# Optimization experiments

Measured on AMD Instinct MI355X. Metric: run time of the kernel, lower is better.

## Reference

```python
import jax, jax.numpy as jnp
import numpy as np

B, T, LA, L = 4, 32, 32, 512
D, H, C = 2048, 16, 128
KV_DIM = 2048
K = T * LA  # total kv tokens per batch element
EPS = 1e-5


def _ln(x):
    m = jnp.mean(x, axis=-1, keepdims=True)
    v = jnp.var(x, axis=-1, keepdims=True)
    return (x - m) * jax.lax.rsqrt(v + EPS)


def setup_inputs() -> dict:
    key = jax.random.key(0)
    ks = jax.random.split(key, 10)
    s = 1.0 / np.sqrt(D)
    sk = 1.0 / np.sqrt(KV_DIM)
    return {
        "x": jax.random.normal(ks[0], (B, T, LA, KV_DIM), jnp.float32),
        "latents": jax.random.normal(ks[1], (B, L, D), jnp.float32),
        "t_emb": jax.random.normal(ks[2], (B, 3, D), jnp.float32) * 0.02,
        "q_lens": jnp.full((B,), L, dtype=jnp.int32),
        "k_lens": jax.random.randint(ks[3], (B,), K // 2, K + 1).astype(jnp.int32),
        "ln_kv_w": jnp.ones((KV_DIM,), jnp.float32),
        "ln_kv_b": jnp.zeros((KV_DIM,), jnp.float32),
        "ssg": jax.random.normal(ks[4], (1, 3, D), jnp.float32) * s,  # shift_scale_gate param (adaLN=True)
        "Wq": jax.random.normal(ks[5], (D, D), jnp.float32) * s,
        "bq": jnp.zeros((D,), jnp.float32),
        "Wkv": jax.random.normal(ks[6], (KV_DIM, 2 * D), jnp.float32) * sk,
        "bkv": jnp.zeros((2 * D,), jnp.float32),
        "Wo": jax.random.normal(ks[7], (D, D), jnp.float32) * s,
        "bo": jnp.zeros((D,), jnp.float32),
    }


def reference(x, latents, t_emb, q_lens, k_lens, ln_kv_w, ln_kv_b, ssg,
              Wq, bq, Wkv, bkv, Wo, bo):
    # norm_kv (affine LayerNorm over kv_dim)
    xk = _ln(x) * ln_kv_w + ln_kv_b  # (B,T,LA,KV_DIM)
    # AdaLN modulate: shift/scale/gate from t_emb + learned shift_scale_gate
    mod = t_emb + ssg  # (B,3,D)
    shift, scale, gate = mod[:, 0:1], mod[:, 1:2], mod[:, 2:3]  # (B,1,D)
    norm_q = _ln(latents)  # norm_q has no affine when adaLN=True
    lat = norm_q * (1.0 + scale) + shift
    # projections
    q = (lat @ Wq + bq).reshape(B, L, H, C)
    kv = (xk.reshape(B, K, KV_DIM) @ Wkv + bkv)  # (B,K,2D)
    k, v = kv[..., :D], kv[..., D:]
    k = k.reshape(B, K, H, C)
    v = v.reshape(B, K, H, C)
    # varlen attention == per-batch masked attention (keys beyond k_lens masked)
    scores = jnp.einsum("blhc,bkhc->bhlk", q, k) / np.sqrt(C)
    kmask = jnp.arange(K)[None, :] < k_lens[:, None]  # (B,K)
    scores = jnp.where(kmask[:, None, None, :], scores, jnp.finfo(scores.dtype).min)
    attn = jax.nn.softmax(scores, axis=-1)
    out = jnp.einsum("bhlk,bkhc->blhc", attn, v).reshape(B, L, D)
    # queries beyond q_lens are invalid -> zero them (varlen packing semantics)
    qmask = (jnp.arange(L)[None, :] < q_lens[:, None])[..., None]  # (B,L,1)
    out = out * qmask
    return (out @ Wo + bo) * gate
```

## Files before the change

kernel.cpp:

```cpp
#include <hip/hip_runtime.h>

typedef unsigned short u16;
typedef short bf16x8 __attribute__((ext_vector_type(8)));
typedef float f32x4 __attribute__((ext_vector_type(4)));

#define MFMA_BF16(a, b, c) __builtin_amdgcn_mfma_f32_16x16x32_bf16((a), (b), (c), 0, 0, 0)
#define ATT_SCALE 0.08838834764831845f

__device__ __forceinline__ u16 f2bf(float f) {
  union { float f; unsigned int u; } cv;
  cv.f = f;
  unsigned int u = cv.u + 0x7fffu + ((cv.u >> 16) & 1u);
  return (u16)(u >> 16);
}

__device__ __forceinline__ void gload_lds16(const u16* g, u16* l) {
  __builtin_amdgcn_global_load_lds(
      (const __attribute__((address_space(1))) unsigned int*)g,
      (__attribute__((address_space(3))) unsigned int*)l, 16, 0, 0);
}

__global__ __launch_bounds__(256) void prep_kernel(
    const float* __restrict__ x, const float* __restrict__ ln_w,
    const float* __restrict__ ln_b, const float* __restrict__ latents,
    const float* __restrict__ t_emb, const float* __restrict__ ssg,
    const float* __restrict__ Wq, const float* __restrict__ Wo,
    const float* __restrict__ Wkv,
    u16* __restrict__ xk_out, u16* __restrict__ lat_out,
    u16* __restrict__ WqT, u16* __restrict__ WoT, u16* __restrict__ WkvT)
{
  __shared__ float shmem[32 * 33];
  const int blk = blockIdx.x;
  const int tid = threadIdx.x;
  if (blk < 6144) {
    const bool is_x = blk < 4096;
    const int row = is_x ? blk : blk - 4096;
    const float* src = is_x ? (x + (size_t)row * 2048) : (latents + (size_t)row * 2048);
    const float4* xr = (const float4*)src;
    float4 v0 = xr[tid];
    float4 v1 = xr[tid + 256];
    float sum = v0.x + v0.y + v0.z + v0.w + v1.x + v1.y + v1.z + v1.w;
    float sq  = v0.x*v0.x + v0.y*v0.y + v0.z*v0.z + v0.w*v0.w
              + v1.x*v1.x + v1.y*v1.y + v1.z*v1.z + v1.w*v1.w;
    #pragma unroll
    for (int off = 32; off > 0; off >>= 1) {
      sum += __shfl_xor(sum, off);
      sq  += __shfl_xor(sq, off);
    }
    if ((tid & 63) == 0) { shmem[tid >> 6] = sum; shmem[(tid >> 6) + 4] = sq; }
    __syncthreads();
    sum = shmem[0] + shmem[1] + shmem[2] + shmem[3];
    sq  = shmem[4] + shmem[5] + shmem[6] + shmem[7];
    const float mean = sum * (1.0f / 2048.0f);
    const float var  = sq * (1.0f / 2048.0f) - mean * mean;
    const float rstd = rsqrtf(var + 1e-5f);
    if (is_x) {
      const float4* w4 = (const float4*)ln_w;
      const float4* b4 = (const float4*)ln_b;
      ushort4* orow = (ushort4*)(xk_out + (size_t)row * 2048);
      #pragma unroll
      for (int j = 0; j < 2; ++j) {
        const int idx = tid + j * 256;
        const float4 v = j ? v1 : v0;
        const float4 ww = w4[idx];
        const float4 bb = b4[idx];
        ushort4 o;
        o.x = f2bf((v.x - mean) * rstd * ww.x + bb.x);
        o.y = f2bf((v.y - mean) * rstd * ww.y + bb.y);
        o.z = f2bf((v.z - mean) * rstd * ww.z + bb.z);
        o.w = f2bf((v.w - mean) * rstd * ww.w + bb.w);
        orow[idx] = o;
      }
    } else {
      const int bidx = row >> 9;
      const float4* te = (const float4*)(t_emb + (size_t)bidx * 3 * 2048);
      const float4* sg = (const float4*)ssg;
      ushort4* orow = (ushort4*)(lat_out + (size_t)row * 2048);
      #pragma unroll
      for (int j = 0; j < 2; ++j) {
        const int idx = tid + j * 256;
        const float4 v = j ? v1 : v0;
        const float4 t0 = te[idx];
        const float4 t1 = te[512 + idx];
        const float4 s0 = sg[idx];
        const float4 s1 = sg[512 + idx];
        ushort4 o;
        o.x = f2bf(((v.x - mean) * rstd) * (1.0f + t1.x + s1.x) + (t0.x + s0.x));
        o.y = f2bf(((v.y - mean) * rstd) * (1.0f + t1.y + s1.y) + (t0.y + s0.y));
        o.z = f2bf(((v.z - mean) * rstd) * (1.0f + t1.z + s1.z) + (t0.z + s0.z));
        o.w = f2bf(((v.w - mean) * rstd) * (1.0f + t1.w + s1.w) + (t0.w + s0.w));
        orow[idx] = o;
      }
    }
  } else {
    int t = blk - 6144;
    const float* in;
    u16* outp;
    int C, cx, ry;
    if (t < 4096)      { in = Wq;  outp = WqT;  C = 2048; cx = t & 63;  ry = t >> 6; }
    else if (t < 8192) { t -= 4096; in = Wo;  outp = WoT;  C = 2048; cx = t & 63;  ry = t >> 6; }
    else               { t -= 8192; in = Wkv; outp = WkvT; C = 4096; cx = t & 127; ry = t >> 7; }
    float (*tile)[33] = (float(*)[33])shmem;
    const int R = 2048;
    const int c0 = cx * 32;
    const int r0 = ry * 32;
    const int tx = tid & 31;
    const int ty = tid >> 5;
    #pragma unroll
    for (int i = 0; i < 4; ++i)
      tile[ty + i * 8][tx] = in[(size_t)(r0 + ty + i * 8) * C + c0 + tx];
    __syncthreads();
    #pragma unroll
    for (int i = 0; i < 4; ++i)
      outp[(size_t)(c0 + ty + i * 8) * R + r0 + tx] = f2bf(tile[tx][ty + i * 8]);
  }
}

template<int BM>
__global__ __launch_bounds__(256) void gemm_bf16_kernel(
    const u16* __restrict__ A, const u16* __restrict__ BT,
    int Kd, int mode,
    const float* __restrict__ bias,
    u16* __restrict__ out_q, float* __restrict__ out_f,
    const float* __restrict__ t_emb, const float* __restrict__ ssg)
{
  constexpr int TI = BM / 32;
  __shared__ u16 As[2][BM][40];
  __shared__ u16 Bs[2][128][40];
  const int tid  = threadIdx.x;
  const int lane = tid & 63;
  const int wv   = tid >> 6;
  const int wm   = wv & 1, wn = wv >> 1;
  const int quad = lane >> 4, lq = lane & 15;
  const int m0 = blockIdx.y * BM, n0 = blockIdx.x * 128;

  f32x4 acc[TI][4];
  #pragma unroll
  for (int i = 0; i < TI; ++i)
    #pragma unroll
    for (int j = 0; j < 4; ++j)
      acc[i][j] = (f32x4){0.f, 0.f, 0.f, 0.f};

  const int rB  = tid >> 1;
  const int hfB = (tid & 1) * 16;
  const u16* gB = BT + (size_t)(n0 + rB) * Kd + hfB;
  const int rA  = (BM == 128) ? (tid >> 1) : (tid >> 2);
  const int hA  = (BM == 128) ? 0 : ((tid >> 1) & 1);
  const int hfA = (tid & 1) * 16;
  const u16* gA = A + (size_t)(m0 + rA) * Kd + hA * 32 + hfA;

  for (int k0 = 0; k0 < Kd; k0 += 64) {
    uint4 a00, a01;
    a00 = *(const uint4*)(gA + k0);
    a01 = *(const uint4*)(gA + k0 + 8);
    const uint4 b00 = *(const uint4*)(gB + k0);
    const uint4 b01 = *(const uint4*)(gB + k0 + 8);
    const uint4 b10 = *(const uint4*)(gB + k0 + 32);
    const uint4 b11 = *(const uint4*)(gB + k0 + 40);
    __syncthreads();
    *(uint4*)&As[hA][rA][hfA]     = a00;
    *(uint4*)&As[hA][rA][hfA + 8] = a01;
    *(uint4*)&Bs[0][rB][hfB]     = b00;
    *(uint4*)&Bs[0][rB][hfB + 8] = b01;
    *(uint4*)&Bs[1][rB][hfB]     = b10;
    *(uint4*)&Bs[1][rB][hfB + 8] = b11;
    __syncthreads();
    #pragma unroll
    for (int kk = 0; kk < 2; ++kk) {
      bf16x8 av[TI], bv[4];
      #pragma unroll
      for (int i = 0; i < TI; ++i)
        av[i] = *(const bf16x8*)&As[kk][wm * (BM / 2) + i * 16 + lq][quad * 8];
      #pragma unroll
      for (int j = 0; j < 4; ++j)
        bv[j] = *(const bf16x8*)&Bs[kk][wn * 64 + j * 16 + lq][quad * 8];
      #pragma unroll
      for (int i = 0; i < TI; ++i)
        #pragma unroll
        for (int j = 0; j < 4; ++j)
          acc[i][j] = MFMA_BF16(av[i], bv[j], acc[i][j]);
    }
  }

  #pragma unroll
  for (int i = 0; i < TI; ++i) {
    const int mlb = m0 + wm * (BM / 2) + i * 16 + quad * 4;
    #pragma unroll
    for (int j = 0; j < 4; ++j) {
      const int n = n0 + wn * 64 + j * 16 + lq;
      const float bs = bias[n];
      if (mode == 0) {
        const int h = n >> 7, c = n & 127;
        #pragma unroll
        for (int rr = 0; rr < 4; ++rr) {
          const int m = mlb + rr;
          const int bb = m >> 9, l = m & 511;
          out_q[((size_t)(bb * 16 + h) * 512 + l) * 128 + c] =
              f2bf((acc[i][j][rr] + bs) * ATT_SCALE);
        }
      } else {
        #pragma unroll
        for (int rr = 0; rr < 4; ++rr) {
          const int m = mlb + rr;
          const int bb = m >> 9;
          const float g = t_emb[((size_t)bb * 3 + 2) * 2048 + n] + ssg[2 * 2048 + n];
          out_f[(size_t)m * 2048 + n] = (acc[i][j][rr] + bs) * g;
        }
      }
    }
  }
}

#define KV_BARRIER() asm volatile("s_barrier" ::: "memory")

#define KV_MMA(MH, NH, BV)                                                     \
  do {                                                                         \
    _Pragma("unroll")                                                          \
    for (int i = 0; i < 4; ++i) {                                              \
      _Pragma("unroll")                                                        \
      for (int j = 0; j < 2; ++j) {                                            \
        acc[(MH)*4 + i][(NH)*2 + j] =                                          \
            MFMA_BF16(av[i][0], BV[j][0], acc[(MH)*4 + i][(NH)*2 + j]);        \
        acc[(MH)*4 + i][(NH)*2 + j] =                                          \
            MFMA_BF16(av[i][1], BV[j][1], acc[(MH)*4 + i][(NH)*2 + j]);        \
      }                                                                        \
    }                                                                          \
  } while (0)

__global__ __launch_bounds__(512, 2) void gemm_kv_8phase(
    const u16* __restrict__ A, const u16* __restrict__ BT,
    const float* __restrict__ bias,
    u16* __restrict__ out_k, u16* __restrict__ out_vT,
    const int* __restrict__ k_lens)
{
  extern __shared__ __align__(16) u16 lds[];
  u16* const Alds = lds;
  u16* const Blds = lds + 32768;

  const int tid  = threadIdx.x;
  const int lane = tid & 63;
  const int wv   = tid >> 6;
  const int wm   = wv >> 2;
  const int wn   = wv & 3;
  const int quad = lane >> 4, lq = lane & 15;
  const int m0 = blockIdx.y * 256, n0 = blockIdx.x * 256;

  f32x4 acc[8][4];
  #pragma unroll
  for (int a = 0; a < 8; ++a)
    #pragma unroll
    for (int b = 0; b < 4; ++b)
      acc[a][b] = (f32x4){0.f, 0.f, 0.f, 0.f};

  const int kl = k_lens[m0 >> 10];
  const bool active = (m0 & 1023) < kl;

  if (active) {
    const int l3 = lane >> 3;
    const int sgcol = (((lane & 7) - l3) & 7) * 8;
    auto stageA = [&](int buf, int mh, int k0) {
      #pragma unroll
      for (int p = 0; p < 2; ++p) {
        const u16* src = A + (size_t)(m0 + p * 128 + mh * 64 + wv * 8 + l3) * 2048 + k0 + sgcol;
        gload_lds16(src, &Alds[(buf * 2 + mh) * 8192 + (p * 8 + wv) * 512]);
      }
    };
    auto stageB = [&](int buf, int nh, int k0) {
      #pragma unroll
      for (int p = 0; p < 2; ++p) {
        const int c = p * 8 + wv;
        const u16* src = BT + (size_t)(n0 + (c >> 2) * 64 + nh * 32 + (c & 3) * 8 + l3) * 2048 + k0 + sgcol;
        gload_lds16(src, &Blds[(buf * 2 + nh) * 8192 + c * 512]);
      }
    };

    bf16x8 av[4][2], bv0[2][2], bv1[2][2];
    const int posk0 = (quad + (lq & 7)) & 7;
    const int posk1 = (4 + quad + (lq & 7)) & 7;
    auto read_av = [&](int buf, int mh) {
      #pragma unroll
      for (int i = 0; i < 4; ++i) {
        const int base = (buf * 2 + mh) * 8192 + (wm * 64 + i * 16 + lq) * 64;
        av[i][0] = *(const bf16x8*)&Alds[base + posk0 * 8];
        av[i][1] = *(const bf16x8*)&Alds[base + posk1 * 8];
      }
    };
    auto read_bv = [&](int buf, int nh, bf16x8 (*bv)[2]) {
      #pragma unroll
      for (int j = 0; j < 2; ++j) {
        const int base = (buf * 2 + nh) * 8192 + (wn * 32 + j * 16 + lq) * 64;
        bv[j][0] = *(const bf16x8*)&Blds[base + posk0 * 8];
        bv[j][1] = *(const bf16x8*)&Blds[base + posk1 * 8];
      }
    };

    const int nt = 32;
    stageA(0, 0, 0); stageB(0, 0, 0); stageA(0, 1, 0); stageB(0, 1, 0);
    stageA(1, 0, 64); stageB(1, 0, 64); stageA(1, 1, 64);
    asm volatile("s_waitcnt vmcnt(6)" ::: "memory");
    KV_BARRIER();

    for (int t = 0; t < nt; ++t) {
      const int cur = t & 1, nxt = cur ^ 1;
      read_av(cur, 0);
      read_bv(cur, 0, bv0);
      if (t + 1 < nt) stageB(nxt, 1, (t + 1) * 64);
      KV_BARRIER();
      __builtin_amdgcn_s_setprio(1);
      KV_MMA(0, 0, bv0);
      __builtin_amdgcn_s_setprio(0);
      KV_BARRIER();
      read_bv(cur, 1, bv1);
      if (t + 2 < nt) stageA(cur, 0, (t + 2) * 64);
      KV_BARRIER();
      __builtin_amdgcn_s_setprio(1);
      KV_MMA(0, 1, bv1);
      __builtin_amdgcn_s_setprio(0);
      KV_BARRIER();
      read_av(cur, 1);
      if (t + 2 < nt) stageB(cur, 0, (t + 2) * 64);
      KV_BARRIER();
      __builtin_amdgcn_s_setprio(1);
      KV_MMA(1, 0, bv0);
      __builtin_amdgcn_s_setprio(0);
      KV_BARRIER();
      if (t + 2 < nt) stageA(cur, 1, (t + 2) * 64);
      KV_BARRIER();
      __builtin_amdgcn_s_setprio(1);
      KV_MMA(1, 1, bv1);
      __builtin_amdgcn_s_setprio(0);
      if (t < nt - 2) {
        asm volatile("s_waitcnt vmcnt(6)" ::: "memory");
      } else if (t == nt - 2) {
        asm volatile("s_waitcnt vmcnt(0)" ::: "memory");
      }
      KV_BARRIER();
    }
  }

  #pragma unroll
  for (int a = 0; a < 8; ++a) {
    const int mlb = m0 + wm * 128 + (a >> 2) * 64 + (a & 3) * 16 + quad * 4;
    #pragma unroll
    for (int b = 0; b < 4; ++b) {
      const int n = n0 + wn * 64 + (b >> 1) * 32 + (b & 1) * 16 + lq;
      const float bs = bias[n];
      if (n < 2048) {
        const int h = n >> 7, c = n & 127;
        #pragma unroll
        for (int rr = 0; rr < 4; ++rr) {
          const int m = mlb + rr;
          const int bb = m >> 10, kk = m & 1023;
          out_k[((size_t)(bb * 16 + h) * 1024 + kk) * 128 + c] = f2bf(acc[a][b][rr] + bs);
        }
      } else {
        const int n2 = n - 2048;
        const int h = n2 >> 7, c = n2 & 127;
        const int bb = mlb >> 10, kk = mlb & 1023;
        ushort4 o4;
        o4.x = f2bf(acc[a][b][0] + bs);
        o4.y = f2bf(acc[a][b][1] + bs);
        o4.z = f2bf(acc[a][b][2] + bs);
        o4.w = f2bf(acc[a][b][3] + bs);
        *(ushort4*)&out_vT[((size_t)(bb * 16 + h) * 128 + c) * 1024 + kk] = o4;
      }
    }
  }
}

__global__ __launch_bounds__(256) void attn_kernel(
    const u16* __restrict__ qb, const u16* __restrict__ kb,
    const u16* __restrict__ vT, const int* __restrict__ k_lens,
    const int* __restrict__ q_lens, u16* __restrict__ ao)
{
  __shared__ u16 Ks[64][132];
  __shared__ u16 Vs[128][68];
  __shared__ u16 Ps[64][68];
  const int tid  = threadIdx.x;
  const int w    = tid >> 6;
  const int lane = tid & 63;
  const int quad = lane >> 4, lq = lane & 15;
  const int bh = blockIdx.x;
  const int b  = bh >> 4;
  const int l0 = blockIdx.y * 64;
  const int kl = k_lens[b];
  const int ql = q_lens[b];

  bf16x8 qf[4];
  {
    const u16* qp = qb + ((size_t)bh * 512 + l0 + w * 16 + lq) * 128 + quad * 8;
    #pragma unroll
    for (int ks = 0; ks < 4; ++ks)
      qf[ks] = *(const bf16x8*)(qp + ks * 32);
  }

  const int krow = tid >> 4;
  const int kcol = tid & 15;
  const u16* kg = kb + ((size_t)bh * 1024 + krow) * 128 + kcol * 8;
  const int vrow = tid >> 3;
  const int vcol = tid & 7;
  const u16* vg = vT + (size_t)bh * 128 * 1024 + (size_t)vrow * 1024 + vcol * 8;

  f32x4 o[8];
  #pragma unroll
  for (int j = 0; j < 8; ++j) o[j] = (f32x4){0.f, 0.f, 0.f, 0.f};
  float mrun[4], lrun[4];
  #pragma unroll
  for (int rr = 0; rr < 4; ++rr) { mrun[rr] = -__builtin_inff(); lrun[rr] = 0.f; }

  const int nkt = (kl + 63) >> 6;
  uint4 kd[4], vd[4];
  #pragma unroll
  for (int p = 0; p < 4; ++p)
    kd[p] = *(const uint4*)(kg + (size_t)(p * 16) * 128);
  #pragma unroll
  for (int p = 0; p < 4; ++p)
    vd[p] = *(const uint4*)(vg + (size_t)p * 32 * 1024);

  for (int kt = 0; kt < nkt; ++kt) {
    __syncthreads();
    #pragma unroll
    for (int p = 0; p < 4; ++p)
      *(uint4*)&Ks[krow + p * 16][kcol * 8] = kd[p];
    #pragma unroll
    for (int p = 0; p < 4; ++p)
      *(uint4*)&Vs[vrow + p * 32][vcol * 8] = vd[p];
    __syncthreads();

    if (kt + 1 < nkt) {
      const int kn = (kt + 1) * 64;
      #pragma unroll
      for (int p = 0; p < 4; ++p)
        kd[p] = *(const uint4*)(kg + (size_t)(kn + p * 16) * 128);
      #pragma unroll
      for (int p = 0; p < 4; ++p)
        vd[p] = *(const uint4*)(vg + (size_t)p * 32 * 1024 + kn);
    }

    const int k0 = kt * 64;
    f32x4 s[4];
    #pragma unroll
    for (int ct = 0; ct < 4; ++ct) {
      s[ct] = (f32x4){0.f, 0.f, 0.f, 0.f};
      #pragma unroll
      for (int ks = 0; ks < 4; ++ks) {
        const bf16x8 kf = *(const bf16x8*)&Ks[ct * 16 + lq][ks * 32 + quad * 8];
        s[ct] = MFMA_BF16(qf[ks], kf, s[ct]);
      }
    }
    #pragma unroll
    for (int ct = 0; ct < 4; ++ct) {
      const bool valid = (k0 + ct * 16 + lq) < kl;
      #pragma unroll
      for (int rr = 0; rr < 4; ++rr)
        s[ct][rr] = valid ? s[ct][rr] : -__builtin_inff();
    }
    float mnew[4], alpha[4], rs[4];
    #pragma unroll
    for (int rr = 0; rr < 4; ++rr) {
      float tm = fmaxf(fmaxf(s[0][rr], s[1][rr]), fmaxf(s[2][rr], s[3][rr]));
      tm = fmaxf(tm, __shfl_xor(tm, 1));
      tm = fmaxf(tm, __shfl_xor(tm, 2));
      tm = fmaxf(tm, __shfl_xor(tm, 4));
      tm = fmaxf(tm, __shfl_xor(tm, 8));
      const float mn = fmaxf(mrun[rr], tm);
      alpha[rr] = __expf(mrun[rr] - mn);
      mrun[rr] = mn;
      mnew[rr] = mn;
      rs[rr] = 0.f;
    }
    #pragma unroll
    for (int ct = 0; ct < 4; ++ct)
      #pragma unroll
      for (int rr = 0; rr < 4; ++rr) {
        const float p = __expf(s[ct][rr] - mnew[rr]);
        s[ct][rr] = p;
        rs[rr] += p;
      }
    #pragma unroll
    for (int rr = 0; rr < 4; ++rr) {
      float t = rs[rr];
      t += __shfl_xor(t, 1);
      t += __shfl_xor(t, 2);
      t += __shfl_xor(t, 4);
      t += __shfl_xor(t, 8);
      lrun[rr] = lrun[rr] * alpha[rr] + t;
    }
    #pragma unroll
    for (int j = 0; j < 8; ++j)
      #pragma unroll
      for (int rr = 0; rr < 4; ++rr)
        o[j][rr] *= alpha[rr];

    #pragma unroll
    for (int ct = 0; ct < 4; ++ct)
      #pragma unroll
      for (int rr = 0; rr < 4; ++rr)
        Ps[w * 16 + quad * 4 + rr][ct * 16 + lq] = f2bf(s[ct][rr]);

    bf16x8 pf[2];
    pf[0] = *(const bf16x8*)&Ps[w * 16 + lq][quad * 8];
    pf[1] = *(const bf16x8*)&Ps[w * 16 + lq][32 + quad * 8];

    #pragma unroll
    for (int j = 0; j < 8; ++j) {
      #pragma unroll
      for (int kk = 0; kk < 2; ++kk) {
        const bf16x8 vf = *(const bf16x8*)&Vs[j * 16 + lq][kk * 32 + quad * 8];
        o[j] = MFMA_BF16(pf[kk], vf, o[j]);
      }
    }
  }

  const int h = bh & 15;
  #pragma unroll
  for (int rr = 0; rr < 4; ++rr) {
    const int row = l0 + w * 16 + quad * 4 + rr;
    const float inv = (row < ql) ? (1.0f / lrun[rr]) : 0.0f;
    u16* op = ao + ((size_t)b * 512 + row) * 2048 + h * 128 + lq;
    #pragma unroll
    for (int j = 0; j < 8; ++j)
      op[j * 16] = f2bf(o[j][rr] * inv);
  }
}

extern "C" void kernel_launch(void* const* d_in, const int* in_sizes, int n_in,
                              void* d_out, int out_size, void* d_ws, size_t ws_size,
                              hipStream_t stream) {
  (void)in_sizes; (void)n_in; (void)out_size; (void)ws_size;
  const float* x       = (const float*)d_in[0];
  const float* latents = (const float*)d_in[1];
  const float* t_emb   = (const float*)d_in[2];
  const int*   q_lens  = (const int*)d_in[3];
  const int*   k_lens  = (const int*)d_in[4];
  const float* ln_w    = (const float*)d_in[5];
  const float* ln_b    = (const float*)d_in[6];
  const float* ssg     = (const float*)d_in[7];
  const float* Wq      = (const float*)d_in[8];
  const float* bq      = (const float*)d_in[9];
  const float* Wkv     = (const float*)d_in[10];
  const float* bkv     = (const float*)d_in[11];
  const float* Wo      = (const float*)d_in[12];
  const float* bo      = (const float*)d_in[13];
  float* out = (float*)d_out;

  u16* ws = (u16*)d_ws;
  const size_t MEG = (size_t)1 << 20;
  u16* WqT  = ws;
  u16* WoT  = ws + 4  * MEG;
  u16* WkvT = ws + 8  * MEG;
  u16* xk   = ws + 16 * MEG;
  u16* lat  = ws + 24 * MEG;
  u16* qb   = ws + 28 * MEG;
  u16* kbuf = ws + 32 * MEG;
  u16* vTb  = ws + 40 * MEG;
  u16* aob  = ws + 48 * MEG;

  hipFuncSetAttribute(reinterpret_cast<const void*>(&gemm_kv_8phase),
                      hipFuncAttributeMaxDynamicSharedMemorySize, 131072);

  prep_kernel<<<dim3(22528), dim3(256), 0, stream>>>(
      x, ln_w, ln_b, latents, t_emb, ssg, Wq, Wo, Wkv,
      xk, lat, WqT, WoT, WkvT);

  gemm_bf16_kernel<64><<<dim3(16, 32), dim3(256), 0, stream>>>(
      lat, WqT, 2048, 0, bq, qb, nullptr, nullptr, nullptr);
  gemm_kv_8phase<<<dim3(16, 16), dim3(512), 131072, stream>>>(
      xk, WkvT, bkv, kbuf, vTb, k_lens);

  attn_kernel<<<dim3(64, 8), dim3(256), 0, stream>>>(qb, kbuf, vTb, k_lens, q_lens, aob);

  gemm_bf16_kernel<64><<<dim3(16, 32), dim3(256), 0, stream>>>(
      aob, WoT, 2048, 2, bo, nullptr, out, t_emb, ssg);
}
```

Baseline: 382.8 us.

## Read K/V fragments directly from global memory in attention, drop LDS staging

The attention kernel stops staging K and V tiles through shared memory with block-wide barriers. Each wave now loads its MFMA K and V fragments straight from global memory, relying on L2 and L1 for reuse. Blocks shrink to two waves covering 32 query rows, and the grid doubles. The output is staged through LDS so each lane writes 16-byte contiguous rows. This removes the __syncthreads and LDS traffic, but each wave now re-reads K/V from cache with no software prefetch, so global load latency is exposed.

```diff
diff --git a/kernel.cpp b/kernel.cpp
--- a/kernel.cpp
+++ b/kernel.cpp
@@ -368,38 +368,33 @@
   }
 }
 
-__global__ __launch_bounds__(256) void attn_kernel(
+__global__ __launch_bounds__(128) void attn_kernel(
     const u16* __restrict__ qb, const u16* __restrict__ kb,
     const u16* __restrict__ vT, const int* __restrict__ k_lens,
     const int* __restrict__ q_lens, u16* __restrict__ ao)
 {
-  __shared__ u16 Ks[64][132];
-  __shared__ u16 Vs[128][68];
-  __shared__ u16 Ps[64][68];
+  __shared__ u16 Ps[2][16][68];
+  __shared__ u16 Os[2][16][136];
   const int tid  = threadIdx.x;
   const int w    = tid >> 6;
   const int lane = tid & 63;
   const int quad = lane >> 4, lq = lane & 15;
   const int bh = blockIdx.x;
   const int b  = bh >> 4;
-  const int l0 = blockIdx.y * 64;
+  const int l0 = blockIdx.y * 32 + w * 16;
   const int kl = k_lens[b];
   const int ql = q_lens[b];
 
   bf16x8 qf[4];
   {
-    const u16* qp = qb + ((size_t)bh * 512 + l0 + w * 16 + lq) * 128 + quad * 8;
+    const u16* qp = qb + ((size_t)bh * 512 + l0 + lq) * 128 + quad * 8;
     #pragma unroll
     for (int ks = 0; ks < 4; ++ks)
       qf[ks] = *(const bf16x8*)(qp + ks * 32);
   }
 
-  const int krow = tid >> 4;
-  const int kcol = tid & 15;
-  const u16* kg = kb + ((size_t)bh * 1024 + krow) * 128 + kcol * 8;
-  const int vrow = tid >> 3;
-  const int vcol = tid & 7;
-  const u16* vg = vT + (size_t)bh * 128 * 1024 + (size_t)vrow * 1024 + vcol * 8;
+  const u16* kgb = kb + (size_t)bh * 1024 * 128;
+  const u16* vgb = vT + (size_t)bh * 128 * 1024;
 
   f32x4 o[8];
   #pragma unroll
@@ -409,42 +404,16 @@
   for (int rr = 0; rr < 4; ++rr) { mrun[rr] = -__builtin_inff(); lrun[rr] = 0.f; }
 
   const int nkt = (kl + 63) >> 6;
-  uint4 kd[4], vd[4];
-  #pragma unroll
-  for (int p = 0; p < 4; ++p)
-    kd[p] = *(const uint4*)(kg + (size_t)(p * 16) * 128);
-  #pragma unroll
-  for (int p = 0; p < 4; ++p)
-    vd[p] = *(const uint4*)(vg + (size_t)p * 32 * 1024);
-
   for (int kt = 0; kt < nkt; ++kt) {
-    __syncthreads();
-    #pragma unroll
-    for (int p = 0; p < 4; ++p)
-      *(uint4*)&Ks[krow + p * 16][kcol * 8] = kd[p];
-    #pragma unroll
-    for (int p = 0; p < 4; ++p)
-      *(uint4*)&Vs[vrow + p * 32][vcol * 8] = vd[p];
-    __syncthreads();
-
-    if (kt + 1 < nkt) {
-      const int kn = (kt + 1) * 64;
-      #pragma unroll
-      for (int p = 0; p < 4; ++p)
-        kd[p] = *(const uint4*)(kg + (size_t)(kn + p * 16) * 128);
-      #pragma unroll
-      for (int p = 0; p < 4; ++p)
-        vd[p] = *(const uint4*)(vg + (size_t)p * 32 * 1024 + kn);
-    }
-
     const int k0 = kt * 64;
+
     f32x4 s[4];
     #pragma unroll
     for (int ct = 0; ct < 4; ++ct) {
       s[ct] = (f32x4){0.f, 0.f, 0.f, 0.f};
       #pragma unroll
       for (int ks = 0; ks < 4; ++ks) {
-        const bf16x8 kf = *(const bf16x8*)&Ks[ct * 16 + lq][ks * 32 + quad * 8];
+        const bf16x8 kf = *(const bf16x8*)(kgb + (size_t)(k0 + ct * 16 + lq) * 128 + ks * 32 + quad * 8);
         s[ct] = MFMA_BF16(qf[ks], kf, s[ct]);
       }
     }
@@ -496,17 +465,17 @@
     for (int ct = 0; ct < 4; ++ct)
       #pragma unroll
       for (int rr = 0; rr < 4; ++rr)
-        Ps[w * 16 + quad * 4 + rr][ct * 16 + lq] = f2bf(s[ct][rr]);
+        Ps[w][quad * 4 + rr][ct * 16 + lq] = f2bf(s[ct][rr]);
 
     bf16x8 pf[2];
-    pf[0] = *(const bf16x8*)&Ps[w * 16 + lq][quad * 8];
-    pf[1] = *(const bf16x8*)&Ps[w * 16 + lq][32 + quad * 8];
+    pf[0] = *(const bf16x8*)&Ps[w][lq][quad * 8];
+    pf[1] = *(const bf16x8*)&Ps[w][lq][32 + quad * 8];
 
     #pragma unroll
     for (int j = 0; j < 8; ++j) {
       #pragma unroll
       for (int kk = 0; kk < 2; ++kk) {
-        const bf16x8 vf = *(const bf16x8*)&Vs[j * 16 + lq][kk * 32 + quad * 8];
+        const bf16x8 vf = *(const bf16x8*)(vgb + (size_t)(j * 16 + lq) * 1024 + k0 + kk * 32 + quad * 8);
         o[j] = MFMA_BF16(pf[kk], vf, o[j]);
       }
     }
@@ -515,12 +484,20 @@
   const int h = bh & 15;
   #pragma unroll
   for (int rr = 0; rr < 4; ++rr) {
-    const int row = l0 + w * 16 + quad * 4 + rr;
+    const int row = l0 + quad * 4 + rr;
     const float inv = (row < ql) ? (1.0f / lrun[rr]) : 0.0f;
-    u16* op = ao + ((size_t)b * 512 + row) * 2048 + h * 128 + lq;
     #pragma unroll
     for (int j = 0; j < 8; ++j)
-      op[j * 16] = f2bf(o[j][rr] * inv);
+      Os[w][quad * 4 + rr][j * 16 + lq] = f2bf(o[j][rr] * inv);
+  }
+  #pragma unroll
+  for (int p = 0; p < 4; ++p) {
+    const int lr = p * 4 + quad;
+    ushort4 lo = *(const ushort4*)&Os[w][lr][lq * 8];
+    ushort4 hi = *(const ushort4*)&Os[w][lr][lq * 8 + 4];
+    u16* op = ao + ((size_t)b * 512 + l0 + lr) * 2048 + h * 128 + lq * 8;
+    *(ushort4*)op = lo;
+    *(ushort4*)(op + 4) = hi;
   }
 }
 
@@ -568,7 +545,7 @@
   gemm_kv_8phase<<<dim3(16, 16), dim3(512), 131072, stream>>>(
       xk, WkvT, bkv, kbuf, vTb, k_lens);
 
-  attn_kernel<<<dim3(64, 8), dim3(256), 0, stream>>>(qb, kbuf, vTb, k_lens, q_lens, aob);
+  attn_kernel<<<dim3(64, 16), dim3(128), 0, stream>>>(qb, kbuf, vTb, k_lens, q_lens, aob);
 
   gemm_bf16_kernel<64><<<dim3(16, 32), dim3(256), 0, stream>>>(
       aob, WoT, 2048, 2, bo, nullptr, out, t_emb, ssg);
```

Result: slower. 407.0 us (+6.3%).
